# Kernel optimization log

Hardware: AMD Instinct MI355X
Metric: run time of the kernel (lower is better)

The kernel has to match this reference:

```python
import jax, jax.numpy as jnp
import numpy as np

B = 1024
C = 256
NUM_CLASSES = 64
MARGIN = 1.0
EPS = 1e-6  # torch F.pairwise_distance default eps, added to the difference


def setup_inputs() -> dict:
    key = jax.random.key(0)
    k1, k2 = jax.random.split(key)
    logits = jax.random.normal(k1, (B, C), dtype=jnp.float32)
    labels = jax.random.randint(k2, (B,), 0, NUM_CLASSES, dtype=jnp.int64)
    return {"logits": logits, "labels": labels}


def reference(logits, labels):
    b = logits.shape[0]
    idx = jnp.arange(b)
    valid = idx[None, :] != idx[:, None]                      # [B,B] off-diagonal
    same = labels[None, :] == labels[:, None]                 # [B,B]
    same_mask = (same & valid).astype(logits.dtype)
    not_same_mask = (~same & valid).astype(logits.dtype)

    # torch: pairwise_distance(logits, logits.unsqueeze(-2)) -> broadcast [B,B,C],
    # dist[i,j] = || logits[j] - logits[i] + eps ||_2
    diff = logits[None, :, :] - logits[:, None, :] + EPS       # [B,B,C]
    dists = jnp.sqrt(jnp.sum(diff * diff, axis=-1))            # [B,B]

    mdists = jnp.maximum(jnp.asarray(MARGIN, logits.dtype) - dists,
                         jnp.asarray(0.0, logits.dtype))

    loss = jnp.sum(dists ** 2 * same_mask + mdists ** 2 * not_same_mask)
    return loss / valid.sum().astype(logits.dtype)
```

## Files before the change

### kernel.cpp

```cpp
#include <hip/hip_runtime.h>
#include <hip/hip_bf16.h>

#define BSZ 1024
#define CDIM 256
#define NVALID 1047552.0

typedef short bf16x8 __attribute__((ext_vector_type(8)));
typedef float f32x16 __attribute__((ext_vector_type(16)));

__global__ __launch_bounds__(256, 1) void cl_main_kernel(
    const float* __restrict__ X, const int* __restrict__ labels,
    double* __restrict__ partials)
{
    const int t    = threadIdx.x;
    const int w    = t >> 6;
    const int lane = t & 63;
    const int lr   = lane & 31;
    const int hi   = lane >> 5;

    const int rbase = blockIdx.y * 64 + (w >> 1) * 32;
    const int cbase = blockIdx.x * 64 + (w & 1) * 32;

    const float* Ap = X + (rbase + lr) * CDIM + hi * 8;
    const float* Bp = X + (cbase + lr) * CDIM + hi * 8;

    const int labA = labels[rbase + lr];
    const int labB = labels[cbase + lr];

    f32x16 dot = {};
    float nA = 0.0f, nB = 0.0f;

#pragma unroll
    for (int s = 0; s < 16; ++s) {
        float4 a0 = *reinterpret_cast<const float4*>(Ap + s * 16);
        float4 a1 = *reinterpret_cast<const float4*>(Ap + s * 16 + 4);
        float4 b0 = *reinterpret_cast<const float4*>(Bp + s * 16);
        float4 b1 = *reinterpret_cast<const float4*>(Bp + s * 16 + 4);

        nA = fmaf(a0.x, a0.x, nA); nA = fmaf(a0.y, a0.y, nA);
        nA = fmaf(a0.z, a0.z, nA); nA = fmaf(a0.w, a0.w, nA);
        nA = fmaf(a1.x, a1.x, nA); nA = fmaf(a1.y, a1.y, nA);
        nA = fmaf(a1.z, a1.z, nA); nA = fmaf(a1.w, a1.w, nA);
        nB = fmaf(b0.x, b0.x, nB); nB = fmaf(b0.y, b0.y, nB);
        nB = fmaf(b0.z, b0.z, nB); nB = fmaf(b0.w, b0.w, nB);
        nB = fmaf(b1.x, b1.x, nB); nB = fmaf(b1.y, b1.y, nB);
        nB = fmaf(b1.z, b1.z, nB); nB = fmaf(b1.w, b1.w, nB);

        union { bf16x8 v; __hip_bfloat162 h[4]; } au, bu;
        au.h[0] = __float22bfloat162_rn(make_float2(a0.x, a0.y));
        au.h[1] = __float22bfloat162_rn(make_float2(a0.z, a0.w));
        au.h[2] = __float22bfloat162_rn(make_float2(a1.x, a1.y));
        au.h[3] = __float22bfloat162_rn(make_float2(a1.z, a1.w));
        bu.h[0] = __float22bfloat162_rn(make_float2(b0.x, b0.y));
        bu.h[1] = __float22bfloat162_rn(make_float2(b0.z, b0.w));
        bu.h[2] = __float22bfloat162_rn(make_float2(b1.x, b1.y));
        bu.h[3] = __float22bfloat162_rn(make_float2(b1.z, b1.w));

        dot = __builtin_amdgcn_mfma_f32_32x32x16_bf16(au.v, bu.v, dot, 0, 0, 0);
    }

    nA += __shfl_xor(nA, 32);
    nB += __shfl_xor(nB, 32);

    const int j = cbase + lr;
    float local = 0.0f;
#pragma unroll
    for (int r = 0; r < 16; ++r) {
        int xrow = (r & 3) + 8 * (r >> 2) + 4 * hi;
        int i = rbase + xrow;
        float rmI = __shfl(nA, xrow);
        int   li  = __shfl(labA, xrow);
        float d2 = fmaxf(rmI + nB - 2.0f * dot[r], 0.0f);
        float dist = sqrtf(d2);
        float m = fmaxf(1.0f - dist, 0.0f);
        float c = (li == labB) ? d2 : m * m;
        if (i != j) local += c;
    }

    for (int off = 32; off; off >>= 1) local += __shfl_xor(local, off);
    if (lane == 0) {
        int widx = (blockIdx.y * 16 + blockIdx.x) * 4 + w;
        partials[widx] = (double)local;
    }
}

__global__ __launch_bounds__(256) void cl_final_kernel(
    const double* __restrict__ p, float* __restrict__ out)
{
    __shared__ double ws4[4];
    int t = threadIdx.x;
    double s = p[t] + p[t + 256] + p[t + 512] + p[t + 768];
    for (int off = 32; off; off >>= 1) s += __shfl_xor(s, off);
    if ((t & 63) == 0) ws4[t >> 6] = s;
    __syncthreads();
    if (t == 0) out[0] = (float)((ws4[0] + ws4[1] + ws4[2] + ws4[3]) / NVALID);
}

extern "C" void kernel_launch(void* const* d_in, const int* in_sizes, int n_in,
                              void* d_out, int out_size, void* d_ws, size_t ws_size,
                              hipStream_t stream)
{
    const float* X      = (const float*)d_in[0];
    const int*   labels = (const int*)d_in[1];
    float*       out    = (float*)d_out;
    double*      partials = (double*)d_ws;

    cl_main_kernel<<<dim3(16, 16), 256, 0, stream>>>(X, labels, partials);
    cl_final_kernel<<<1, 256, 0, stream>>>(partials, out);
}
```

Baseline: 16.43 us.

## Fuse final reduction into main kernel via cooperative grid sync

Merges the two-kernel design into one cooperative launch. Each block writes its per-wave partials with atomic stores, waits on a grid-wide barrier, and block 0 then performs the final reduction. This removes the second kernel launch and its dispatch gap, at the cost of the grid-sync overhead and the cooperative-launch requirement. It also adds an odd no-op fmaf on the norm accumulation that contributes zero.

```diff
diff --git a/kernel.cpp b/kernel.cpp
--- a/kernel.cpp
+++ b/kernel.cpp
@@ -1,5 +1,6 @@
 #include <hip/hip_runtime.h>
 #include <hip/hip_bf16.h>
+#include <hip/hip_cooperative_groups.h>
 
 #define BSZ 1024
 #define CDIM 256
@@ -8,9 +9,9 @@
 typedef short bf16x8 __attribute__((ext_vector_type(8)));
 typedef float f32x16 __attribute__((ext_vector_type(16)));
 
-__global__ __launch_bounds__(256, 1) void cl_main_kernel(
+__global__ __launch_bounds__(256, 1) void cl_coop_kernel(
     const float* __restrict__ X, const int* __restrict__ labels,
-    double* __restrict__ partials)
+    double* __restrict__ partials, float* __restrict__ out)
 {
     const int t    = threadIdx.x;
     const int w    = t >> 6;
@@ -18,8 +19,10 @@
     const int lr   = lane & 31;
     const int hi   = lane >> 5;
 
-    const int rbase = blockIdx.y * 64 + (w >> 1) * 32;
-    const int cbase = blockIdx.x * 64 + (w & 1) * 32;
+    const int bx = blockIdx.x & 15;
+    const int by = blockIdx.x >> 4;
+    const int rbase = by * 64 + (w >> 1) * 32;
+    const int cbase = bx * 64 + (w & 1) * 32;
 
     const float* Ap = X + (rbase + lr) * CDIM + hi * 8;
     const float* Bp = X + (cbase + lr) * CDIM + hi * 8;
@@ -42,6 +45,7 @@
         nA = fmaf(a1.x, a1.x, nA); nA = fmaf(a1.y, a1.y, nA);
         nA = fmaf(a1.z, a1.z, nA); nA = fmaf(a1.w, a1.w, nA);
         nB = fmaf(b0.x, b0.x, nB); nB = fmaf(b0.y, b0.y, nB);
+        nB = fmaf(b0.y * 0.0f + b0.y, 0.0f, nB);
         nB = fmaf(b0.z, b0.z, nB); nB = fmaf(b0.w, b0.w, nB);
         nB = fmaf(b1.x, b1.x, nB); nB = fmaf(b1.y, b1.y, nB);
         nB = fmaf(b1.z, b1.z, nB); nB = fmaf(b1.w, b1.w, nB);
@@ -79,32 +83,36 @@
 
     for (int off = 32; off; off >>= 1) local += __shfl_xor(local, off);
     if (lane == 0) {
-        int widx = (blockIdx.y * 16 + blockIdx.x) * 4 + w;
-        partials[widx] = (double)local;
+        __hip_atomic_store(&partials[blockIdx.x * 4 + w], (double)local,
+                           __ATOMIC_RELAXED, __HIP_MEMORY_SCOPE_AGENT);
     }
-}
 
-__global__ __launch_bounds__(256) void cl_final_kernel(
-    const double* __restrict__ p, float* __restrict__ out)
-{
-    __shared__ double ws4[4];
-    int t = threadIdx.x;
-    double s = p[t] + p[t + 256] + p[t + 512] + p[t + 768];
-    for (int off = 32; off; off >>= 1) s += __shfl_xor(s, off);
-    if ((t & 63) == 0) ws4[t >> 6] = s;
-    __syncthreads();
-    if (t == 0) out[0] = (float)((ws4[0] + ws4[1] + ws4[2] + ws4[3]) / NVALID);
+    cooperative_groups::this_grid().sync();
+
+    if (blockIdx.x == 0) {
+        __shared__ double ws4[4];
+        double s = 0.0;
+#pragma unroll
+        for (int q = 0; q < 4; ++q)
+            s += __hip_atomic_load(&partials[t + q * 256],
+                                   __ATOMIC_RELAXED, __HIP_MEMORY_SCOPE_AGENT);
+        for (int off = 32; off; off >>= 1) s += __shfl_xor(s, off);
+        if ((t & 63) == 0) ws4[t >> 6] = s;
+        __syncthreads();
+        if (t == 0) out[0] = (float)((ws4[0] + ws4[1] + ws4[2] + ws4[3]) / NVALID);
+    }
 }
 
 extern "C" void kernel_launch(void* const* d_in, const int* in_sizes, int n_in,
                               void* d_out, int out_size, void* d_ws, size_t ws_size,
                               hipStream_t stream)
 {
-    const float* X      = (const float*)d_in[0];
-    const int*   labels = (const int*)d_in[1];
-    float*       out    = (float*)d_out;
+    const float* X        = (const float*)d_in[0];
+    const int*   labels   = (const int*)d_in[1];
+    float*       out      = (float*)d_out;
     double*      partials = (double*)d_ws;
 
-    cl_main_kernel<<<dim3(16, 16), 256, 0, stream>>>(X, labels, partials);
-    cl_final_kernel<<<1, 256, 0, stream>>>(partials, out);
+    void* args[] = {(void*)&X, (void*)&labels, (void*)&partials, (void*)&out};
+    hipLaunchCooperativeKernel((const void*)cl_coop_kernel,
+                               dim3(256), dim3(256), args, 0, stream);
 }
```

Measured after the change: 48.31 us. 194% more time.
